# Performance work log

Hardware: AMD Instinct MI355X
Metric: run time of the kernel (lower is better)

## Reference

```python
import jax, jax.numpy as jnp
import numpy as np
import math

HEADS = 32
DIM_HEAD = 64
DM = HEADS * DIM_HEAD  # 2048
B, S = 2, 1024
BITS = 3
N_LEVELS = 2 ** BITS
N_GROUPS = (DIM_HEAD + 2) // 3  # 22
PAD = (3 - DIM_HEAD % 3) % 3    # 2
EPS_NORM = 1e-8
EPS_RMS = 1e-6


def _rotors_to_matrices(r):
    # r: (G,4) unit rotors [s, b12, b13, b23] -> (G,3,3) rotation matrices
    s, p, q, rr = r[:, 0], r[:, 1], r[:, 2], r[:, 3]
    s2, p2, q2, r2 = s * s, p * p, q * q, rr * rr
    M = np.zeros((r.shape[0], 3, 3), dtype=np.float32)
    M[:, 0, 0] = s2 - p2 - q2 + r2
    M[:, 0, 1] = 2 * s * p - 2 * q * rr
    M[:, 0, 2] = 2 * s * q + 2 * p * rr
    M[:, 1, 0] = -2 * s * p - 2 * q * rr
    M[:, 1, 1] = s2 - p2 + q2 - r2
    M[:, 1, 2] = 2 * s * rr - 2 * p * q
    M[:, 2, 0] = -2 * s * q + 2 * p * rr
    M[:, 2, 1] = -2 * s * rr - 2 * p * q
    M[:, 2, 2] = s2 + p2 - q2 - r2
    return M


def _make_compressor(seed):
    rng = np.random.default_rng(seed)
    rot = rng.standard_normal((N_GROUPS, 4)).astype(np.float32)
    rot /= np.linalg.norm(rot, axis=-1, keepdims=True)
    M = _rotors_to_matrices(rot)
    sigma = 1.0 / math.sqrt(DIM_HEAD)  # Lloyd-Max for N(0, 1/d)
    C = np.linspace(-3 * sigma, 3 * sigma, N_LEVELS, dtype=np.float32)
    return jnp.asarray(M), jnp.asarray(np.ascontiguousarray(M.transpose(0, 2, 1))), jnp.asarray(C)


def setup_inputs() -> dict:
    key = jax.random.key(0)
    ks = jax.random.split(key, 8)
    x = jax.random.normal(ks[0], (B, S, DM), dtype=jnp.float32)
    w_scale = 0.02
    Wq = jax.random.normal(ks[1], (DM, DM), dtype=jnp.float32) * w_scale
    Wk = jax.random.normal(ks[2], (DM, DM), dtype=jnp.float32) * w_scale
    Wv = jax.random.normal(ks[3], (DM, DM), dtype=jnp.float32) * w_scale
    Wo = jax.random.normal(ks[4], (DM, DM), dtype=jnp.float32) * w_scale
    qn_w = jnp.ones((DM,), dtype=jnp.float32)
    kn_w = jnp.ones((DM,), dtype=jnp.float32)
    Mk, Mtk, Ck = _make_compressor(42)
    Mv, Mtv, Cv = _make_compressor(4200)
    return {"x": x, "Wq": Wq, "Wk": Wk, "Wv": Wv, "Wo": Wo,
            "qn_w": qn_w, "kn_w": kn_w,
            "Mk": Mk, "Mtk": Mtk, "Ck": Ck,
            "Mv": Mv, "Mtv": Mtv, "Cv": Cv}


def _rmsnorm(x, w):
    return x * jax.lax.rsqrt(jnp.mean(x * x, axis=-1, keepdims=True) + EPS_RMS) * w


def _quant_roundtrip(h, M, Mt, C):
    """RotorQuant compress+decompress. h: (B,H,S,Dh) -> (B,H,S,Dh)."""
    norms = jnp.maximum(jnp.linalg.norm(h, axis=-1, keepdims=True), EPS_NORM)
    xu = h / norms
    xu = jnp.pad(xu, ((0, 0), (0, 0), (0, 0), (0, PAD)))
    g = xu.reshape(h.shape[0], h.shape[1], h.shape[2], N_GROUPS, 3)
    rot = jnp.einsum('bhsgi,gij->bhsgj', g, M)
    flat = rot.reshape(h.shape[0], h.shape[1], h.shape[2], N_GROUPS * 3)
    # nearest-centroid quantization (uint8 indices in original)
    idx = jnp.argmin(jnp.abs(flat[..., None] - C), axis=-1)
    deq = C[idx]
    g2 = deq.reshape(h.shape[0], h.shape[1], h.shape[2], N_GROUPS, 3)
    der = jnp.einsum('bhsgi,gij->bhsgj', g2, Mt)
    out = der.reshape(h.shape[0], h.shape[1], h.shape[2], N_GROUPS * 3)[..., :DIM_HEAD]
    return out * norms


def reference(x, Wq, Wk, Wv, Wo, qn_w, kn_w, Mk, Mtk, Ck, Mv, Mtv, Cv):
    b, s, _ = x.shape
    v = x @ Wv
    q = _rmsnorm(x @ Wq, qn_w)
    k = _rmsnorm(x @ Wk, kn_w)
    # split heads -> (B,H,S,Dh)
    qh = q.reshape(b, s, HEADS, DIM_HEAD).transpose(0, 2, 1, 3)
    kh = k.reshape(b, s, HEADS, DIM_HEAD).transpose(0, 2, 1, 3)
    vh = v.reshape(b, s, HEADS, DIM_HEAD).transpose(0, 2, 1, 3)
    # per-head rotor quantization roundtrip of K and V
    kh = _quant_roundtrip(kh, Mk, Mtk, Ck)
    vh = _quant_roundtrip(vh, Mv, Mtv, Cv)
    # scaled dot-product attention
    scores = jnp.einsum('bhqd,bhkd->bhqk', qh, kh) / math.sqrt(DIM_HEAD)
    probs = jax.nn.softmax(scores, axis=-1)
    o = jnp.einsum('bhqk,bhkd->bhqd', probs, vh)
    o = o.transpose(0, 2, 1, 3).reshape(b, s, DM)
    return o @ Wo
```

## Files before the change

### kernel.cpp

```cpp
#include <hip/hip_runtime.h>
#include <hip/hip_bf16.h>
#include <math.h>

#define HEADS 32
#define DIM_HEAD 64
#define DM 2048
#define BATCH 2
#define SEQ 1024
#define NROWS (BATCH * SEQ)
#define NVEC (NROWS * HEADS)
#define N_GROUPS 22
#define N_LEVELS 8
#define EPS_NORM 1e-8f
#define EPS_RMS 1e-6f

typedef float f32x4 __attribute__((ext_vector_type(4)));
typedef __bf16 bf16x8 __attribute__((ext_vector_type(8)));
typedef unsigned short u16x8 __attribute__((ext_vector_type(8)));
typedef unsigned short u16x4 __attribute__((ext_vector_type(4)));

__device__ __forceinline__ unsigned short f2bf(float x) {
  union { float f; unsigned u; } v; v.f = x;
  unsigned r = v.u + 0x7fffu + ((v.u >> 16) & 1u);
  return (unsigned short)(r >> 16);
}
__device__ __forceinline__ float bf2f(unsigned short h) {
  union { unsigned u; float f; } v; v.u = ((unsigned)h) << 16;
  return v.f;
}
__device__ __forceinline__ bf16x8 ldfrag(const unsigned short* p) {
  return __builtin_bit_cast(bf16x8, *(const u16x8*)p);
}
#define MFMA16(a, b, c) __builtin_amdgcn_mfma_f32_16x16x32_bf16((a), (b), (c), 0, 0, 0)

__device__ __forceinline__ void stage16(const unsigned short* g, unsigned short* lds) {
  __builtin_amdgcn_global_load_lds(
      (const __attribute__((address_space(1))) unsigned int*)g,
      (__attribute__((address_space(3))) unsigned int*)lds, 16, 0, 0);
}

__global__ __launch_bounds__(256) void split_convert_kernel(
    const float* __restrict__ X, unsigned short* __restrict__ hi,
    unsigned short* __restrict__ lo, int n8) {
  const int i = blockIdx.x * 256 + threadIdx.x;
  if (i >= n8) return;
  const float4 a = ((const float4*)X)[2 * i];
  const float4 b = ((const float4*)X)[2 * i + 1];
  const float v[8] = {a.x, a.y, a.z, a.w, b.x, b.y, b.z, b.w};
  u16x8 h, l;
#pragma unroll
  for (int j = 0; j < 8; ++j) {
    const unsigned short hh = f2bf(v[j]);
    h[j] = hh;
    l[j] = f2bf(v[j] - bf2f(hh));
  }
  ((u16x8*)hi)[i] = h;
  if (lo) ((u16x8*)lo)[i] = l;
}

__global__ __launch_bounds__(256) void transpose_split_batch_kernel(
    const float* __restrict__ W0, const float* __restrict__ W1,
    const float* __restrict__ W2, const float* __restrict__ W3,
    unsigned short* __restrict__ T0h, unsigned short* __restrict__ T1h,
    unsigned short* __restrict__ T1l, unsigned short* __restrict__ T2h,
    unsigned short* __restrict__ T2l, unsigned short* __restrict__ T3h) {
  const int z = blockIdx.z;
  const float* W = (z == 0) ? W0 : (z == 1) ? W1 : (z == 2) ? W2 : W3;
  unsigned short* Th = (z == 0) ? T0h : (z == 1) ? T1h : (z == 2) ? T2h : T3h;
  unsigned short* Tl = (z == 1) ? T1l : (z == 2) ? T2l : nullptr;

  __shared__ float S[64][65];
  const int t = threadIdx.x;
  const int tk = blockIdx.y * 64, tm = blockIdx.x * 64;
  {
    const int r = t >> 2, cs = (t & 3) * 16;
    const float* src = W + (size_t)(tk + r) * DM + tm + cs;
#pragma unroll
    for (int j = 0; j < 16; j += 4) {
      float4 v = *(const float4*)(src + j);
      S[r][cs + j] = v.x; S[r][cs + j + 1] = v.y;
      S[r][cs + j + 2] = v.z; S[r][cs + j + 3] = v.w;
    }
  }
  __syncthreads();
  const int m = t >> 2, ks = (t & 3) * 16;
  u16x8 h0, h1, l0, l1;
#pragma unroll
  for (int j = 0; j < 8; ++j) {
    const float v = S[ks + j][m];
    const unsigned short hh = f2bf(v);
    h0[j] = hh; l0[j] = f2bf(v - bf2f(hh));
  }
#pragma unroll
  for (int j = 0; j < 8; ++j) {
    const float v = S[ks + 8 + j][m];
    const unsigned short hh = f2bf(v);
    h1[j] = hh; l1[j] = f2bf(v - bf2f(hh));
  }
  const size_t o = (size_t)(tm + m) * DM + tk + ks;
  *(u16x8*)&Th[o] = h0; *(u16x8*)&Th[o + 8] = h1;
  if (Tl) { *(u16x8*)&Tl[o] = l0; *(u16x8*)&Tl[o + 8] = l1; }
}

__global__ __launch_bounds__(256) void qkv_gemm_kernel(
    const unsigned short* __restrict__ Ahi, const unsigned short* __restrict__ Alo,
    const unsigned short* __restrict__ Bhi, const unsigned short* __restrict__ Blo,
    float* __restrict__ q, float* __restrict__ k, float* __restrict__ v) {
  __shared__ unsigned short lAhi[128 * 32];
  __shared__ unsigned short lBhi[128 * 32];
  __shared__ unsigned short lAlo[128 * 32];
  __shared__ unsigned short lBlo[128 * 32];

  const int t = threadIdx.x;
  const int lane = t & 63, wave = t >> 6;
  const int wr = wave >> 1, wc = wave & 1;
  const int gm0 = blockIdx.y * 128;
  const int gnc = blockIdx.x * 128;
  const int seg = gnc >> 11;
  const bool split = (seg != 0);
  const int lrsub = lane >> 2;
  const int lcsub = lane & 3;

  f32x4 acc[4][4] = {};

  for (int kt = 0; kt < DM; kt += 32) {
    __syncthreads();
#pragma unroll
    for (int rg = wave; rg < 8; rg += 4) {
      const int lrow = rg * 16 + lrsub;
      const int c = lcsub ^ ((lrow >> 1) & 3);
      const size_t goffA = (size_t)(gm0 + lrow) * DM + kt + c * 8;
      const size_t goffB = (size_t)(gnc + lrow) * DM + kt + c * 8;
      stage16(Ahi + goffA, lAhi + rg * 512);
      stage16(Bhi + goffB, lBhi + rg * 512);
      if (split) {
        stage16(Alo + goffA, lAlo + rg * 512);
        stage16(Blo + goffB, lBlo + rg * 512);
      }
    }
    __syncthreads();

    bf16x8 ah[4], bh[4], al[4], bl[4];
#pragma unroll
    for (int i = 0; i < 4; ++i) {
      const int mrow = wr * 64 + i * 16 + (lane & 15);
      const int offa = mrow * 32 + (((lane >> 4) ^ ((mrow >> 1) & 3)) << 3);
      ah[i] = ldfrag(&lAhi[offa]);
      const int nrow = wc * 64 + i * 16 + (lane & 15);
      const int offb = nrow * 32 + (((lane >> 4) ^ ((nrow >> 1) & 3)) << 3);
      bh[i] = ldfrag(&lBhi[offb]);
      if (split) {
        al[i] = ldfrag(&lAlo[offa]);
        bl[i] = ldfrag(&lBlo[offb]);
      }
    }
#pragma unroll
    for (int i = 0; i < 4; ++i)
#pragma unroll
      for (int j = 0; j < 4; ++j) {
        acc[i][j] = MFMA16(ah[i], bh[j], acc[i][j]);
        if (split) {
          acc[i][j] = MFMA16(ah[i], bl[j], acc[i][j]);
          acc[i][j] = MFMA16(al[i], bh[j], acc[i][j]);
        }
      }
  }

  float* C = (seg == 0) ? q : (seg == 1) ? k : v;
  const int gn0 = gnc & 2047;
#pragma unroll
  for (int i = 0; i < 4; ++i) {
    const int row = gm0 + wr * 64 + i * 16 + ((lane >> 4) << 2);
#pragma unroll
    for (int j = 0; j < 4; ++j) {
      const int col = gn0 + wc * 64 + j * 16 + (lane & 15);
#pragma unroll
      for (int r = 0; r < 4; ++r)
        C[(size_t)(row + r) * DM + col] = acc[i][j][r];
    }
  }
}

__global__ __launch_bounds__(256) void gemm_out_splitk_kernel(
    const unsigned short* __restrict__ Ahi, const unsigned short* __restrict__ Bt,
    float* __restrict__ Cpart) {
  __shared__ unsigned short lAhi[128 * 32];
  __shared__ unsigned short lBhi[128 * 32];

  const int t = threadIdx.x;
  const int lane = t & 63, wave = t >> 6;
  const int wr = wave >> 1, wc = wave & 1;
  const int gm0 = blockIdx.y * 128, gn0 = blockIdx.x * 128;
  const int z = blockIdx.z;
  const int k0 = z * (DM / 2);
  const int lrsub = lane >> 2;
  const int lcsub = lane & 3;

  f32x4 acc[4][4] = {};

  for (int kt = k0; kt < k0 + DM / 2; kt += 32) {
    __syncthreads();
#pragma unroll
    for (int rg = wave; rg < 8; rg += 4) {
      const int lrow = rg * 16 + lrsub;
      const int c = lcsub ^ ((lrow >> 1) & 3);
      stage16(Ahi + (size_t)(gm0 + lrow) * DM + kt + c * 8, lAhi + rg * 512);
      stage16(Bt + (size_t)(gn0 + lrow) * DM + kt + c * 8, lBhi + rg * 512);
    }
    __syncthreads();

    bf16x8 ah[4], bh[4];
#pragma unroll
    for (int i = 0; i < 4; ++i) {
      const int mrow = wr * 64 + i * 16 + (lane & 15);
      ah[i] = ldfrag(&lAhi[mrow * 32 + (((lane >> 4) ^ ((mrow >> 1) & 3)) << 3)]);
      const int nrow = wc * 64 + i * 16 + (lane & 15);
      bh[i] = ldfrag(&lBhi[nrow * 32 + (((lane >> 4) ^ ((nrow >> 1) & 3)) << 3)]);
    }
#pragma unroll
    for (int i = 0; i < 4; ++i)
#pragma unroll
      for (int j = 0; j < 4; ++j)
        acc[i][j] = MFMA16(ah[i], bh[j], acc[i][j]);
  }

  float* C = Cpart + (size_t)z * NROWS * DM;
#pragma unroll
  for (int i = 0; i < 4; ++i) {
    const int row = gm0 + wr * 64 + i * 16 + ((lane >> 4) << 2);
#pragma unroll
    for (int j = 0; j < 4; ++j) {
      const int col = gn0 + wc * 64 + j * 16 + (lane & 15);
#pragma unroll
      for (int r = 0; r < 4; ++r)
        C[(size_t)(row + r) * DM + col] = acc[i][j][r];
    }
  }
}

__global__ __launch_bounds__(256) void add2_f4_kernel(
    const float* __restrict__ a, const float* __restrict__ b,
    float* __restrict__ o, int n4) {
  const int i = blockIdx.x * 256 + threadIdx.x;
  if (i >= n4) return;
  const float4 x = ((const float4*)a)[i];
  const float4 y = ((const float4*)b)[i];
  ((float4*)o)[i] = make_float4(x.x + y.x, x.y + y.y, x.z + y.z, x.w + y.w);
}

__device__ __forceinline__ float wave_sum(float x) {
#pragma unroll
  for (int o = 32; o > 0; o >>= 1) x += __shfl_xor(x, o, 64);
  return x;
}

__global__ __launch_bounds__(256) void rmsnorm_kernel(
    float* __restrict__ y, const float* __restrict__ w) {
  __shared__ float rbuf[4];
  const int row = blockIdx.x;
  float* p = y + (size_t)row * DM;
  const int t = threadIdx.x;
  const int wave = t >> 6, lane = t & 63;

  float ss = 0.f;
#pragma unroll
  for (int c = t; c < DM; c += 256) { float v = p[c]; ss += v * v; }
  ss = wave_sum(ss);
  if (lane == 0) rbuf[wave] = ss;
  __syncthreads();
  ss = rbuf[0] + rbuf[1] + rbuf[2] + rbuf[3];
  const float scale = rsqrtf(ss * (1.0f / DM) + EPS_RMS);
#pragma unroll
  for (int c = t; c < DM; c += 256) p[c] = p[c] * scale * w[c];
}

__global__ __launch_bounds__(256) void rmsnorm_split_kernel(
    const float* __restrict__ y, const float* __restrict__ w,
    unsigned short* __restrict__ hi, unsigned short* __restrict__ lo,
    float post) {
  __shared__ float rbuf[4];
  const int row = blockIdx.x;
  const float* p = y + (size_t)row * DM;
  const int t = threadIdx.x;
  const int wave = t >> 6, lane = t & 63;

  const int c0 = t * 8;
  float4 a = *(const float4*)(p + c0);
  float4 b = *(const float4*)(p + c0 + 4);
  float v[8] = {a.x, a.y, a.z, a.w, b.x, b.y, b.z, b.w};
  float ss = 0.f;
#pragma unroll
  for (int j = 0; j < 8; ++j) ss += v[j] * v[j];
  ss = wave_sum(ss);
  if (lane == 0) rbuf[wave] = ss;
  __syncthreads();
  ss = rbuf[0] + rbuf[1] + rbuf[2] + rbuf[3];
  const float scale = rsqrtf(ss * (1.0f / DM) + EPS_RMS) * post;

  u16x8 hv, lv;
#pragma unroll
  for (int j = 0; j < 8; ++j) {
    const float val = v[j] * scale * w[c0 + j];
    const unsigned short hh = f2bf(val);
    hv[j] = hh; lv[j] = f2bf(val - bf2f(hh));
  }
  *(u16x8*)&hi[(size_t)row * DM + c0] = hv;
  *(u16x8*)&lo[(size_t)row * DM + c0] = lv;
}

__device__ __forceinline__ float qnearest(float v, const float* __restrict__ C) {
  float best = C[0];
  float bd = fabsf(v - C[0]);
#pragma unroll
  for (int i = 1; i < N_LEVELS; ++i) {
    float d = fabsf(v - C[i]);
    if (d < bd) { bd = d; best = C[i]; }
  }
  return best;
}

template <bool WRITE_BF>
__global__ __launch_bounds__(256) void quant_kernel(
    float* __restrict__ kv, const float* __restrict__ M,
    const float* __restrict__ Mt, const float* __restrict__ C,
    unsigned short* __restrict__ hi, unsigned short* __restrict__ lo) {
  const int vec = blockIdx.x * blockDim.x + threadIdx.x;
  if (vec >= NVEC) return;
  float* p = kv + (size_t)vec * DIM_HEAD;

  float h[66];
  float ss = 0.f;
#pragma unroll
  for (int d = 0; d < DIM_HEAD; ++d) { h[d] = p[d]; ss += h[d] * h[d]; }
  float norm = fmaxf(sqrtf(ss), EPS_NORM);
  const float inv = 1.0f / norm;
#pragma unroll
  for (int d = 0; d < DIM_HEAD; ++d) h[d] *= inv;
  h[64] = 0.f; h[65] = 0.f;

#pragma unroll
  for (int g = 0; g < N_GROUPS; ++g) {
    const float* Mg  = M  + g * 9;
    const float* Mtg = Mt + g * 9;
    const float a0 = h[3 * g + 0], a1 = h[3 * g + 1], a2 = h[3 * g + 2];
    const float r0 = a0 * Mg[0] + a1 * Mg[3] + a2 * Mg[6];
    const float r1 = a0 * Mg[1] + a1 * Mg[4] + a2 * Mg[7];
    const float r2 = a0 * Mg[2] + a1 * Mg[5] + a2 * Mg[8];
    const float d0 = qnearest(r0, C);
    const float d1 = qnearest(r1, C);
    const float d2 = qnearest(r2, C);
    h[3 * g + 0] = d0 * Mtg[0] + d1 * Mtg[3] + d2 * Mtg[6];
    h[3 * g + 1] = d0 * Mtg[1] + d1 * Mtg[4] + d2 * Mtg[7];
    h[3 * g + 2] = d0 * Mtg[2] + d1 * Mtg[5] + d2 * Mtg[8];
  }
  if (WRITE_BF) {
#pragma unroll
    for (int g8 = 0; g8 < 8; ++g8) {
      u16x8 hv, lv;
#pragma unroll
      for (int j = 0; j < 8; ++j) {
        const float val = h[g8 * 8 + j] * norm;
        const unsigned short hh = f2bf(val);
        hv[j] = hh; lv[j] = f2bf(val - bf2f(hh));
      }
      *(u16x8*)&hi[(size_t)vec * DIM_HEAD + g8 * 8] = hv;
      *(u16x8*)&lo[(size_t)vec * DIM_HEAD + g8 * 8] = lv;
    }
  } else {
#pragma unroll
    for (int d = 0; d < DIM_HEAD; ++d) p[d] = h[d] * norm;
  }
}

__global__ __launch_bounds__(256) void vt_split_kernel(
    const float* __restrict__ v, unsigned short* __restrict__ hi,
    unsigned short* __restrict__ lo) {
  __shared__ float T[64][65];
  const int s0 = blockIdx.x * 64;
  const int bh = blockIdx.y;
  const int b = bh >> 5, h = bh & 31;
  const int t = threadIdx.x;
  {
    const int sr = t >> 2, dseg = (t & 3) * 16;
    const float* src = v + ((size_t)(b * SEQ + s0 + sr) * DM + h * 64 + dseg);
#pragma unroll
    for (int j = 0; j < 16; j += 4) {
      float4 a = *(const float4*)(src + j);
      T[sr][dseg + j] = a.x; T[sr][dseg + j + 1] = a.y;
      T[sr][dseg + j + 2] = a.z; T[sr][dseg + j + 3] = a.w;
    }
  }
  __syncthreads();
  const int d = t >> 2, sseg = (t & 3) * 16;
  u16x8 h0, h1, l0, l1;
#pragma unroll
  for (int j = 0; j < 8; ++j) {
    const float val = T[sseg + j][d];
    const unsigned short hh = f2bf(val);
    h0[j] = hh; l0[j] = f2bf(val - bf2f(hh));
  }
#pragma unroll
  for (int j = 0; j < 8; ++j) {
    const float val = T[sseg + 8 + j][d];
    const unsigned short hh = f2bf(val);
    h1[j] = hh; l1[j] = f2bf(val - bf2f(hh));
  }
  const size_t o = (size_t)(bh * 64 + d) * SEQ + s0 + sseg;
  *(u16x8*)&hi[o] = h0; *(u16x8*)&hi[o + 8] = h1;
  *(u16x8*)&lo[o] = l0; *(u16x8*)&lo[o + 8] = l1;
}

__global__ __launch_bounds__(256) void attn_mfma_kernel(
    const unsigned short* __restrict__ qhi, const unsigned short* __restrict__ qlo,
    const unsigned short* __restrict__ khi, const unsigned short* __restrict__ klo,
    const unsigned short* __restrict__ vthi, const unsigned short* __restrict__ vtlo,
    unsigned short* __restrict__ ohi) {
  __shared__ unsigned short Ks_h[4096], Ks_l[4096];
  __shared__ unsigned short Vt_h[4096], Vt_l[4096];
  __shared__ unsigned int   Ps[4096];

  const int bh = blockIdx.x;
  const int qt = blockIdx.y;
  const int h = bh & 31, b = bh >> 5;
  const int q0 = qt * 64;
  const int t = threadIdx.x, lane = t & 63, w = t >> 6;
  const int quad = lane >> 4, l15 = lane & 15;
  const int srow = lane >> 3, schunk = lane & 7;

  auto stage = [&](const unsigned short* g, int stride, unsigned short* arr) {
#pragma unroll
    for (int it = 0; it < 2; ++it) {
      const int r = w * 16 + it * 8 + srow;
      const int c = schunk ^ (r & 7);
      stage16(g + (size_t)r * stride + c * 8, arr + (w * 16 + it * 8) * 64);
    }
  };

  bf16x8 qh[2], ql[2];
  {
    const size_t qrow = (size_t)(b * SEQ + q0 + w * 16 + l15) * DM + h * 64;
#pragma unroll
    for (int ks = 0; ks < 2; ++ks) {
      qh[ks] = ldfrag(&qhi[qrow + ks * 32 + quad * 8]);
      ql[ks] = ldfrag(&qlo[qrow + ks * 32 + quad * 8]);
    }
  }

  f32x4 acc[4] = {};
  float m_prev[4] = {-INFINITY, -INFINITY, -INFINITY, -INFINITY};
  float lsum[4] = {0.f, 0.f, 0.f, 0.f};

  const unsigned short* gkh = khi + ((size_t)(b * SEQ) * DM + h * 64);
  const unsigned short* gkl = klo + ((size_t)(b * SEQ) * DM + h * 64);
  const unsigned short* gvh = vthi + (size_t)(bh * 64) * SEQ;
  const unsigned short* gvl = vtlo + (size_t)(bh * 64) * SEQ;

  for (int kt = 0; kt < SEQ; kt += 64) {
    __syncthreads();
    stage(gkh + (size_t)kt * DM, DM, Ks_h);
    stage(gkl + (size_t)kt * DM, DM, Ks_l);
    stage(gvh + kt, SEQ, Vt_h);
    stage(gvl + kt, SEQ, Vt_l);
    __syncthreads();

    f32x4 s[4] = {};
#pragma unroll
    for (int nt = 0; nt < 4; ++nt) {
#pragma unroll
      for (int ks = 0; ks < 2; ++ks) {
        const int row = nt * 16 + l15;
        const int off = row * 64 + (((quad + 4 * ks) ^ (row & 7)) << 3);
        const bf16x8 kh = ldfrag(&Ks_h[off]);
        const bf16x8 kl = ldfrag(&Ks_l[off]);
        s[nt] = MFMA16(qh[ks], kh, s[nt]);
        s[nt] = MFMA16(qh[ks], kl, s[nt]);
        s[nt] = MFMA16(ql[ks], kh, s[nt]);
      }
    }

    float asave[4];
#pragma unroll
    for (int r = 0; r < 4; ++r) {
      float mx = fmaxf(fmaxf(s[0][r], s[1][r]), fmaxf(s[2][r], s[3][r]));
#pragma unroll
      for (int off = 1; off < 16; off <<= 1) mx = fmaxf(mx, __shfl_xor(mx, off, 64));
      const float mn = fmaxf(m_prev[r], mx);
      const float al = __expf(m_prev[r] - mn);
      float rs = 0.f;
#pragma unroll
      for (int nt = 0; nt < 4; ++nt) {
        const float e = __expf(s[nt][r] - mn);
        s[nt][r] = e; rs += e;
      }
#pragma unroll
      for (int off = 1; off < 16; off <<= 1) rs += __shfl_xor(rs, off, 64);
      lsum[r] = lsum[r] * al + rs;
      m_prev[r] = mn;
      asave[r] = al;
      const int prow = w * 16 + quad * 4 + r;
#pragma unroll
      for (int nt = 0; nt < 4; ++nt) {
        const int kk = nt * 16 + l15;
        const unsigned short hh = f2bf(s[nt][r]);
        const unsigned short ll = f2bf(s[nt][r] - bf2f(hh));
        Ps[prow * 64 + (kk ^ ((prow & 7) << 3))] =
            ((unsigned)hh << 16) | (unsigned)ll;
      }
    }

    {
      const int src = (l15 >> 2) << 4;
      const float a0 = __shfl(asave[0], src, 64);
      const float a1 = __shfl(asave[1], src, 64);
      const float a2 = __shfl(asave[2], src, 64);
      const float a3 = __shfl(asave[3], src, 64);
      const int rr = l15 & 3;
      const float alph = (rr == 0) ? a0 : (rr == 1) ? a1 : (rr == 2) ? a2 : a3;
#pragma unroll
      for (int mt = 0; mt < 4; ++mt) acc[mt] *= alph;
    }

    bf16x8 ph[2], pl[2];
#pragma unroll
    for (int ks = 0; ks < 2; ++ks) {
      const int prow = w * 16 + l15;
      const unsigned int* pp =
          &Ps[prow * 64 + ((ks * 32 + quad * 8) ^ ((prow & 7) << 3))];
      const uint4 pa = *(const uint4*)pp;
      const uint4 pb = *(const uint4*)(pp + 4);
      u16x8 hv, lv;
      const unsigned int pw[8] = {pa.x, pa.y, pa.z, pa.w, pb.x, pb.y, pb.z, pb.w};
#pragma unroll
      for (int j = 0; j < 8; ++j) {
        hv[j] = (unsigned short)(pw[j] >> 16);
        lv[j] = (unsigned short)(pw[j] & 0xffffu);
      }
      ph[ks] = __builtin_bit_cast(bf16x8, hv);
      pl[ks] = __builtin_bit_cast(bf16x8, lv);
    }

#pragma unroll
    for (int mt = 0; mt < 4; ++mt) {
#pragma unroll
      for (int ks = 0; ks < 2; ++ks) {
        const int drow = mt * 16 + l15;
        const int offv = drow * 64 + (((quad + 4 * ks) ^ (drow & 7)) << 3);
        const bf16x8 vh = ldfrag(&Vt_h[offv]);
        const bf16x8 vl = ldfrag(&Vt_l[offv]);
        acc[mt] = MFMA16(vh, ph[ks], acc[mt]);
        acc[mt] = MFMA16(vh, pl[ks], acc[mt]);
        acc[mt] = MFMA16(vl, ph[ks], acc[mt]);
      }
    }
  }

  {
    const int src = (l15 >> 2) << 4;
    const float a0 = __shfl(lsum[0], src, 64);
    const float a1 = __shfl(lsum[1], src, 64);
    const float a2 = __shfl(lsum[2], src, 64);
    const float a3 = __shfl(lsum[3], src, 64);
    const int rr = l15 & 3;
    const float lq = (rr == 0) ? a0 : (rr == 1) ? a1 : (rr == 2) ? a2 : a3;
    const float inv = 1.0f / lq;
    const size_t obase = (size_t)(b * SEQ + q0 + w * 16 + l15) * DM + h * 64;
#pragma unroll
    for (int mt = 0; mt < 4; ++mt) {
      u16x4 ov;
#pragma unroll
      for (int r = 0; r < 4; ++r) ov[r] = f2bf(acc[mt][r] * inv);
      *(u16x4*)&ohi[obase + mt * 16 + quad * 4] = ov;
    }
  }
}

extern "C" void kernel_launch(void* const* d_in, const int* in_sizes, int n_in,
                              void* d_out, int out_size, void* d_ws, size_t ws_size,
                              hipStream_t stream) {
  const float* x    = (const float*)d_in[0];
  const float* Wq   = (const float*)d_in[1];
  const float* Wk   = (const float*)d_in[2];
  const float* Wv   = (const float*)d_in[3];
  const float* Wo   = (const float*)d_in[4];
  const float* qn_w = (const float*)d_in[5];
  const float* kn_w = (const float*)d_in[6];
  const float* Mk   = (const float*)d_in[7];
  const float* Mtk  = (const float*)d_in[8];
  const float* Ck   = (const float*)d_in[9];
  const float* Mv   = (const float*)d_in[10];
  const float* Mtv  = (const float*)d_in[11];
  const float* Cv   = (const float*)d_in[12];
  float* out = (float*)d_out;

  const size_t MBb = 1024ull * 1024ull;
  const size_t SEG = (size_t)DM * DM;
  char* w = (char*)d_ws;
  float* qb = (float*)(w + 0 * MBb);
  float* kb = (float*)(w + 16 * MBb);
  float* vb = (float*)(w + 32 * MBb);
  unsigned short* xhi     = (unsigned short*)(w + 48 * MBb);
  unsigned short* xlo     = (unsigned short*)(w + 56 * MBb);
  unsigned short* wcat_hi = (unsigned short*)(w + 64 * MBb);
  unsigned short* wcat_lo = (unsigned short*)(w + 88 * MBb);
  unsigned short* wot     = (unsigned short*)(w + 112 * MBb);
  unsigned short* q_hi  = wcat_hi;
  unsigned short* k_hi  = wcat_hi + SEG;
  unsigned short* k_lo  = wcat_hi + 2 * SEG;
  unsigned short* q_lo  = wcat_lo;
  unsigned short* vt_hi = wcat_lo + SEG;
  unsigned short* vt_lo = wcat_lo + 2 * SEG;
  unsigned short* o_hi  = xhi;
  float* opart = (float*)(w + 0 * MBb);

  const int n8 = (NROWS * DM) / 8;

  split_convert_kernel<<<n8 / 256, 256, 0, stream>>>(x, xhi, xlo, n8);
  transpose_split_batch_kernel<<<dim3(DM / 64, DM / 64, 4), 256, 0, stream>>>(
      Wq, Wk, Wv, Wo,
      wcat_hi, wcat_hi + SEG, wcat_lo + SEG, wcat_hi + 2 * SEG, wcat_lo + 2 * SEG, wot);

  qkv_gemm_kernel<<<dim3(3 * DM / 128, NROWS / 128), 256, 0, stream>>>(
      xhi, xlo, wcat_hi, wcat_lo, qb, kb, vb);

  rmsnorm_kernel<<<NROWS, 256, 0, stream>>>(kb, kn_w);
  rmsnorm_split_kernel<<<NROWS, 256, 0, stream>>>(qb, qn_w, q_hi, q_lo, 0.125f);

  quant_kernel<true ><<<NVEC / 256, 256, 0, stream>>>(kb, Mk, Mtk, Ck, k_hi, k_lo);
  quant_kernel<false><<<NVEC / 256, 256, 0, stream>>>(vb, Mv, Mtv, Cv, nullptr, nullptr);
  vt_split_kernel<<<dim3(SEQ / 64, BATCH * HEADS), 256, 0, stream>>>(vb, vt_hi, vt_lo);

  attn_mfma_kernel<<<dim3(BATCH * HEADS, SEQ / 64), 256, 0, stream>>>(
      q_hi, q_lo, k_hi, k_lo, vt_hi, vt_lo, o_hi);

  gemm_out_splitk_kernel<<<dim3(DM / 128, NROWS / 128, 2), 256, 0, stream>>>(
      o_hi, wot, opart);
  add2_f4_kernel<<<(NROWS * DM / 4 + 255) / 256, 256, 0, stream>>>(
      opart, opart + (size_t)NROWS * DM, out, NROWS * DM / 4);
}
```

Before: 458.8 us.

## Rewrite QKV and output GEMMs with double-buffered async LDS pipeline and 8 waves

Replaces the QKV and output-projection GEMMs with new kernels that use 512-thread blocks (8 waves), a 64-wide K tile, and double-buffered LDS. The next tile is prefetched with global_load_lds while the current one is computed, using explicit vmcnt waits, barriers and raised wave priority around the MFMA block. The fused QKV launch is split into a plain-bf16 Q GEMM and a separate split-precision K/V GEMM that stages its hi/lo operands in phases. The aim is to hide global-load latency and drop the per-block branching on the split path. The cost is a larger LDS footprint, which may limit occupancy, and hand-written wait counts that must match the loads actually issued.

```diff
diff --git a/kernel.cpp b/kernel.cpp
--- a/kernel.cpp
+++ b/kernel.cpp
@@ -39,6 +39,11 @@
       (__attribute__((address_space(3))) unsigned int*)lds, 16, 0, 0);
 }
 
+#define WAITV(N) asm volatile("s_waitcnt vmcnt(" #N ")" ::: "memory")
+#define WAITL0() asm volatile("s_waitcnt lgkmcnt(0)" ::: "memory")
+#define SBARM()  asm volatile("s_barrier" ::: "memory")
+#define SFENCE() __builtin_amdgcn_sched_barrier(0)
+
 __global__ __launch_bounds__(256) void split_convert_kernel(
     const float* __restrict__ X, unsigned short* __restrict__ hi,
     unsigned short* __restrict__ lo, int n8) {
@@ -102,135 +107,176 @@
   if (Tl) { *(u16x8*)&Tl[o] = l0; *(u16x8*)&Tl[o + 8] = l1; }
 }
 
-__global__ __launch_bounds__(256) void qkv_gemm_kernel(
-    const unsigned short* __restrict__ Ahi, const unsigned short* __restrict__ Alo,
-    const unsigned short* __restrict__ Bhi, const unsigned short* __restrict__ Blo,
-    float* __restrict__ q, float* __restrict__ k, float* __restrict__ v) {
-  __shared__ unsigned short lAhi[128 * 32];
-  __shared__ unsigned short lBhi[128 * 32];
-  __shared__ unsigned short lAlo[128 * 32];
-  __shared__ unsigned short lBlo[128 * 32];
-
-  const int t = threadIdx.x;
-  const int lane = t & 63, wave = t >> 6;
-  const int wr = wave >> 1, wc = wave & 1;
+__global__ __launch_bounds__(512, 2) void gemm_plain8(
+    const unsigned short* __restrict__ A, const unsigned short* __restrict__ B,
+    float* __restrict__ C, int ntiles) {
+  __shared__ unsigned short L[2][2][128 * 64];
+  const int t = threadIdx.x, lane = t & 63, w = t >> 6;
+  const int wr = w >> 2, wc = w & 3;
   const int gm0 = blockIdx.y * 128;
-  const int gnc = blockIdx.x * 128;
-  const int seg = gnc >> 11;
-  const bool split = (seg != 0);
-  const int lrsub = lane >> 2;
-  const int lcsub = lane & 3;
-
-  f32x4 acc[4][4] = {};
-
-  for (int kt = 0; kt < DM; kt += 32) {
-    __syncthreads();
-#pragma unroll
-    for (int rg = wave; rg < 8; rg += 4) {
-      const int lrow = rg * 16 + lrsub;
-      const int c = lcsub ^ ((lrow >> 1) & 3);
-      const size_t goffA = (size_t)(gm0 + lrow) * DM + kt + c * 8;
-      const size_t goffB = (size_t)(gnc + lrow) * DM + kt + c * 8;
-      stage16(Ahi + goffA, lAhi + rg * 512);
-      stage16(Bhi + goffB, lBhi + rg * 512);
-      if (split) {
-        stage16(Alo + goffA, lAlo + rg * 512);
-        stage16(Blo + goffB, lBlo + rg * 512);
-      }
-    }
-    __syncthreads();
-
-    bf16x8 ah[4], bh[4], al[4], bl[4];
-#pragma unroll
-    for (int i = 0; i < 4; ++i) {
-      const int mrow = wr * 64 + i * 16 + (lane & 15);
-      const int offa = mrow * 32 + (((lane >> 4) ^ ((mrow >> 1) & 3)) << 3);
-      ah[i] = ldfrag(&lAhi[offa]);
-      const int nrow = wc * 64 + i * 16 + (lane & 15);
-      const int offb = nrow * 32 + (((lane >> 4) ^ ((nrow >> 1) & 3)) << 3);
-      bh[i] = ldfrag(&lBhi[offb]);
-      if (split) {
-        al[i] = ldfrag(&lAlo[offa]);
-        bl[i] = ldfrag(&lBlo[offb]);
-      }
-    }
+  const int gn0 = blockIdx.x * 128;
+  const int z = blockIdx.z;
+  const int k0 = z * (ntiles << 6);
+  const int chunk = (lane & 7) ^ (lane >> 3);
+
+  auto stg = [&](const unsigned short* g, int row0, int kt, unsigned short* dst) {
+#pragma unroll
+    for (int it = 0; it < 2; ++it) {
+      const int r = (w << 4) + (it << 3) + (lane >> 3);
+      stage16(g + (size_t)(row0 + r) * DM + kt + chunk * 8,
+              dst + ((w << 4) + (it << 3)) * 64);
+    }
+  };
+
+  f32x4 acc[4][2] = {};
+
+  stg(A, gm0, k0, L[0][0]);
+  stg(B, gn0, k0, L[0][1]);
+
+  for (int tt = 0; tt < ntiles; ++tt) {
+    const int c = tt & 1, n = c ^ 1;
+    const bool pf = (tt + 1 < ntiles);
+    if (pf) {
+      const int ktn = k0 + ((tt + 1) << 6);
+      stg(A, gm0, ktn, L[n][0]);
+      stg(B, gn0, ktn, L[n][1]);
+      WAITV(4);
+    } else {
+      WAITV(0);
+    }
+    SBARM(); SFENCE();
+    const unsigned short* cA = L[c][0];
+    const unsigned short* cB = L[c][1];
+    bf16x8 fa[4][2], fb[2][2];
+#pragma unroll
+    for (int ks = 0; ks < 2; ++ks) {
+      const int ch = ks * 4 + (lane >> 4);
+#pragma unroll
+      for (int i = 0; i < 4; ++i) {
+        const int row = wr * 64 + i * 16 + (lane & 15);
+        fa[i][ks] = ldfrag(&cA[row * 64 + ((ch ^ (row & 7)) << 3)]);
+      }
+#pragma unroll
+      for (int j = 0; j < 2; ++j) {
+        const int row = wc * 32 + j * 16 + (lane & 15);
+        fb[j][ks] = ldfrag(&cB[row * 64 + ((ch ^ (row & 7)) << 3)]);
+      }
+    }
+    WAITL0();
+    __builtin_amdgcn_s_setprio(1);
 #pragma unroll
     for (int i = 0; i < 4; ++i)
 #pragma unroll
-      for (int j = 0; j < 4; ++j) {
-        acc[i][j] = MFMA16(ah[i], bh[j], acc[i][j]);
-        if (split) {
-          acc[i][j] = MFMA16(ah[i], bl[j], acc[i][j]);
-          acc[i][j] = MFMA16(al[i], bh[j], acc[i][j]);
-        }
-      }
-  }
-
-  float* C = (seg == 0) ? q : (seg == 1) ? k : v;
-  const int gn0 = gnc & 2047;
+      for (int j = 0; j < 2; ++j)
+#pragma unroll
+        for (int ks = 0; ks < 2; ++ks)
+          acc[i][j] = MFMA16(fa[i][ks], fb[j][ks], acc[i][j]);
+    __builtin_amdgcn_s_setprio(0);
+    SFENCE(); SBARM();
+  }
+
+  float* Cz = C + (size_t)z * NROWS * DM;
 #pragma unroll
   for (int i = 0; i < 4; ++i) {
     const int row = gm0 + wr * 64 + i * 16 + ((lane >> 4) << 2);
 #pragma unroll
-    for (int j = 0; j < 4; ++j) {
-      const int col = gn0 + wc * 64 + j * 16 + (lane & 15);
+    for (int j = 0; j < 2; ++j) {
+      const int col = gn0 + wc * 32 + j * 16 + (lane & 15);
 #pragma unroll
       for (int r = 0; r < 4; ++r)
-        C[(size_t)(row + r) * DM + col] = acc[i][j][r];
-    }
-  }
-}
-
-__global__ __launch_bounds__(256) void gemm_out_splitk_kernel(
-    const unsigned short* __restrict__ Ahi, const unsigned short* __restrict__ Bt,
-    float* __restrict__ Cpart) {
-  __shared__ unsigned short lAhi[128 * 32];
-  __shared__ unsigned short lBhi[128 * 32];
-
-  const int t = threadIdx.x;
-  const int lane = t & 63, wave = t >> 6;
-  const int wr = wave >> 1, wc = wave & 1;
-  const int gm0 = blockIdx.y * 128, gn0 = blockIdx.x * 128;
-  const int z = blockIdx.z;
-  const int k0 = z * (DM / 2);
-  const int lrsub = lane >> 2;
-  const int lcsub = lane & 3;
-
-  f32x4 acc[4][4] = {};
-
-  for (int kt = k0; kt < k0 + DM / 2; kt += 32) {
-    __syncthreads();
-#pragma unroll
-    for (int rg = wave; rg < 8; rg += 4) {
-      const int lrow = rg * 16 + lrsub;
-      const int c = lcsub ^ ((lrow >> 1) & 3);
-      stage16(Ahi + (size_t)(gm0 + lrow) * DM + kt + c * 8, lAhi + rg * 512);
-      stage16(Bt + (size_t)(gn0 + lrow) * DM + kt + c * 8, lBhi + rg * 512);
-    }
-    __syncthreads();
-
-    bf16x8 ah[4], bh[4];
-#pragma unroll
-    for (int i = 0; i < 4; ++i) {
-      const int mrow = wr * 64 + i * 16 + (lane & 15);
-      ah[i] = ldfrag(&lAhi[mrow * 32 + (((lane >> 4) ^ ((mrow >> 1) & 3)) << 3)]);
-      const int nrow = wc * 64 + i * 16 + (lane & 15);
-      bh[i] = ldfrag(&lBhi[nrow * 32 + (((lane >> 4) ^ ((nrow >> 1) & 3)) << 3)]);
-    }
+        Cz[(size_t)(row + r) * DM + col] = acc[i][j][r];
+    }
+  }
+}
+
+__global__ __launch_bounds__(512, 2) void gemm_kv_split8(
+    const unsigned short* __restrict__ Ah, const unsigned short* __restrict__ Al,
+    const unsigned short* __restrict__ Bh, const unsigned short* __restrict__ Bl,
+    float* __restrict__ kout, float* __restrict__ vout) {
+  __shared__ unsigned short L[2][4][128 * 64];
+  const int t = threadIdx.x, lane = t & 63, w = t >> 6;
+  const int wr = w >> 2, wc = w & 3;
+  const int gm0 = blockIdx.y * 128;
+  const int nAbs = 2048 + blockIdx.x * 128;
+  const int seg = nAbs >> 11;
+  const int gn0 = nAbs & 2047;
+  const int chunk = (lane & 7) ^ (lane >> 3);
+
+  auto stg = [&](const unsigned short* g, int row0, int kt, unsigned short* dst) {
+#pragma unroll
+    for (int it = 0; it < 2; ++it) {
+      const int r = (w << 4) + (it << 3) + (lane >> 3);
+      stage16(g + (size_t)(row0 + r) * DM + kt + chunk * 8,
+              dst + ((w << 4) + (it << 3)) * 64);
+    }
+  };
+
+  f32x4 acc[4][2] = {};
+
+  auto group = [&](const unsigned short* arrA, const unsigned short* arrB) {
+    bf16x8 fa[4][2], fb[2][2];
+#pragma unroll
+    for (int ks = 0; ks < 2; ++ks) {
+      const int ch = ks * 4 + (lane >> 4);
+#pragma unroll
+      for (int i = 0; i < 4; ++i) {
+        const int row = wr * 64 + i * 16 + (lane & 15);
+        fa[i][ks] = ldfrag(&arrA[row * 64 + ((ch ^ (row & 7)) << 3)]);
+      }
+#pragma unroll
+      for (int j = 0; j < 2; ++j) {
+        const int row = wc * 32 + j * 16 + (lane & 15);
+        fb[j][ks] = ldfrag(&arrB[row * 64 + ((ch ^ (row & 7)) << 3)]);
+      }
+    }
+    WAITL0();
+    __builtin_amdgcn_s_setprio(1);
 #pragma unroll
     for (int i = 0; i < 4; ++i)
 #pragma unroll
-      for (int j = 0; j < 4; ++j)
-        acc[i][j] = MFMA16(ah[i], bh[j], acc[i][j]);
-  }
-
-  float* C = Cpart + (size_t)z * NROWS * DM;
+      for (int j = 0; j < 2; ++j)
+#pragma unroll
+        for (int ks = 0; ks < 2; ++ks)
+          acc[i][j] = MFMA16(fa[i][ks], fb[j][ks], acc[i][j]);
+    __builtin_amdgcn_s_setprio(0);
+  };
+
+  stg(Ah, gm0, 0, L[0][0]);
+  stg(Bh, nAbs, 0, L[0][1]);
+  stg(Bl, nAbs, 0, L[0][2]);
+  stg(Al, gm0, 0, L[0][3]);
+
+  for (int tt = 0; tt < 32; ++tt) {
+    const int c = tt & 1, n = c ^ 1;
+    const bool pf = (tt + 1 < 32);
+    const int ktn = (tt + 1) << 6;
+
+    if (pf) { stg(Ah, gm0, ktn, L[n][0]); stg(Bh, nAbs, ktn, L[n][1]); WAITV(8); }
+    else WAITV(4);
+    SBARM(); SFENCE();
+    group(L[c][0], L[c][1]);
+    SFENCE(); SBARM();
+
+    if (pf) { stg(Bl, nAbs, ktn, L[n][2]); WAITV(8); }
+    else WAITV(2);
+    SBARM(); SFENCE();
+    group(L[c][0], L[c][2]);
+    SFENCE(); SBARM();
+
+    if (pf) { stg(Al, gm0, ktn, L[n][3]); WAITV(8); }
+    else WAITV(0);
+    SBARM(); SFENCE();
+    group(L[c][3], L[c][1]);
+    SFENCE(); SBARM();
+  }
+
+  float* C = (seg == 1) ? kout : vout;
 #pragma unroll
   for (int i = 0; i < 4; ++i) {
     const int row = gm0 + wr * 64 + i * 16 + ((lane >> 4) << 2);
 #pragma unroll
-    for (int j = 0; j < 4; ++j) {
-      const int col = gn0 + wc * 64 + j * 16 + (lane & 15);
+    for (int j = 0; j < 2; ++j) {
+      const int col = gn0 + wc * 32 + j * 16 + (lane & 15);
 #pragma unroll
       for (int r = 0; r < 4; ++r)
         C[(size_t)(row + r) * DM + col] = acc[i][j][r];
@@ -619,8 +665,10 @@
       Wq, Wk, Wv, Wo,
       wcat_hi, wcat_hi + SEG, wcat_lo + SEG, wcat_hi + 2 * SEG, wcat_lo + 2 * SEG, wot);
 
-  qkv_gemm_kernel<<<dim3(3 * DM / 128, NROWS / 128), 256, 0, stream>>>(
-      xhi, xlo, wcat_hi, wcat_lo, qb, kb, vb);
+  gemm_plain8<<<dim3(DM / 128, NROWS / 128, 1), 512, 0, stream>>>(
+      xhi, wcat_hi, qb, DM / 64);
+  gemm_kv_split8<<<dim3(2 * DM / 128, NROWS / 128), 512, 0, stream>>>(
+      xhi, xlo, wcat_hi, wcat_lo, kb, vb);
 
   rmsnorm_kernel<<<NROWS, 256, 0, stream>>>(kb, kn_w);
   rmsnorm_split_kernel<<<NROWS, 256, 0, stream>>>(qb, qn_w, q_hi, q_lo, 0.125f);
@@ -632,8 +680,8 @@
   attn_mfma_kernel<<<dim3(BATCH * HEADS, SEQ / 64), 256, 0, stream>>>(
       q_hi, q_lo, k_hi, k_lo, vt_hi, vt_lo, o_hi);
 
-  gemm_out_splitk_kernel<<<dim3(DM / 128, NROWS / 128, 2), 256, 0, stream>>>(
-      o_hi, wot, opart);
+  gemm_plain8<<<dim3(DM / 128, NROWS / 128, 2), 512, 0, stream>>>(
+      o_hi, wot, opart, DM / 64 / 2);
   add2_f4_kernel<<<(NROWS * DM / 4 + 255) / 256, 256, 0, stream>>>(
       opart, opart + (size_t)NROWS * DM, out, NROWS * DM / 4);
 }
```

New measurement: 481.9 us. 5.0% more time.

## Double-buffer K/V tiles in attention kernel with async prefetch and setprio

Applied to the files above, without the earlier changes.

The attention kernel now double-buffers the K/V LDS tiles, issuing global_load_lds for the next tile before computing on the current one. Raw s_waitcnt vmcnt and s_barrier replace the two __syncthreads per iteration, with sched_barrier fences around them. s_setprio is raised around the MFMA blocks. The goal is to hide global-load latency behind compute, at the cost of doubling LDS use (about 80KB), which may reduce occupancy. The vmcnt(8) count depends on the exact number of outstanding loads, which makes it fragile.

```diff
diff --git a/kernel.cpp b/kernel.cpp
--- a/kernel.cpp
+++ b/kernel.cpp
@@ -38,6 +38,10 @@
       (const __attribute__((address_space(1))) unsigned int*)g,
       (__attribute__((address_space(3))) unsigned int*)lds, 16, 0, 0);
 }
+
+#define WAITV(N) asm volatile("s_waitcnt vmcnt(" #N ")" ::: "memory")
+#define SBARM()  asm volatile("s_barrier" ::: "memory")
+#define SFENCE() __builtin_amdgcn_sched_barrier(0)
 
 __global__ __launch_bounds__(256) void split_convert_kernel(
     const float* __restrict__ X, unsigned short* __restrict__ hi,
@@ -415,8 +419,8 @@
     const unsigned short* __restrict__ khi, const unsigned short* __restrict__ klo,
     const unsigned short* __restrict__ vthi, const unsigned short* __restrict__ vtlo,
     unsigned short* __restrict__ ohi) {
-  __shared__ unsigned short Ks_h[4096], Ks_l[4096];
-  __shared__ unsigned short Vt_h[4096], Vt_l[4096];
+  __shared__ unsigned short Ks_h[2][4096], Ks_l[2][4096];
+  __shared__ unsigned short Vt_h[2][4096], Vt_l[2][4096];
   __shared__ unsigned int   Ps[4096];
 
   const int bh = blockIdx.x;
@@ -436,47 +440,64 @@
     }
   };
 
-  bf16x8 qh[2], ql[2];
-  {
-    const size_t qrow = (size_t)(b * SEQ + q0 + w * 16 + l15) * DM + h * 64;
-#pragma unroll
-    for (int ks = 0; ks < 2; ++ks) {
-      qh[ks] = ldfrag(&qhi[qrow + ks * 32 + quad * 8]);
-      ql[ks] = ldfrag(&qlo[qrow + ks * 32 + quad * 8]);
-    }
-  }
-
-  f32x4 acc[4] = {};
-  float m_prev[4] = {-INFINITY, -INFINITY, -INFINITY, -INFINITY};
-  float lsum[4] = {0.f, 0.f, 0.f, 0.f};
-
   const unsigned short* gkh = khi + ((size_t)(b * SEQ) * DM + h * 64);
   const unsigned short* gkl = klo + ((size_t)(b * SEQ) * DM + h * 64);
   const unsigned short* gvh = vthi + (size_t)(bh * 64) * SEQ;
   const unsigned short* gvl = vtlo + (size_t)(bh * 64) * SEQ;
 
-  for (int kt = 0; kt < SEQ; kt += 64) {
-    __syncthreads();
-    stage(gkh + (size_t)kt * DM, DM, Ks_h);
-    stage(gkl + (size_t)kt * DM, DM, Ks_l);
-    stage(gvh + kt, SEQ, Vt_h);
-    stage(gvl + kt, SEQ, Vt_l);
-    __syncthreads();
+  auto stageAll = [&](int kt, int buf) {
+    stage(gkh + (size_t)kt * DM, DM, Ks_h[buf]);
+    stage(gkl + (size_t)kt * DM, DM, Ks_l[buf]);
+    stage(gvh + kt, SEQ, Vt_h[buf]);
+    stage(gvl + kt, SEQ, Vt_l[buf]);
+  };
+
+  bf16x8 qh[2], ql[2];
+  {
+    const size_t qrow = (size_t)(b * SEQ + q0 + w * 16 + l15) * DM + h * 64;
+#pragma unroll
+    for (int ks = 0; ks < 2; ++ks) {
+      qh[ks] = ldfrag(&qhi[qrow + ks * 32 + quad * 8]);
+      ql[ks] = ldfrag(&qlo[qrow + ks * 32 + quad * 8]);
+    }
+  }
+
+  f32x4 acc[4] = {};
+  float m_prev[4] = {-INFINITY, -INFINITY, -INFINITY, -INFINITY};
+  float lsum[4] = {0.f, 0.f, 0.f, 0.f};
+
+  stageAll(0, 0);
+
+  for (int tt = 0; tt < 16; ++tt) {
+    const int c = tt & 1, n = c ^ 1;
+    if (tt < 15) {
+      stageAll((tt + 1) * 64, n);
+      WAITV(8);
+    } else {
+      WAITV(0);
+    }
+    SBARM(); SFENCE();
+    const unsigned short* cKh = Ks_h[c];
+    const unsigned short* cKl = Ks_l[c];
+    const unsigned short* cVh = Vt_h[c];
+    const unsigned short* cVl = Vt_l[c];
 
     f32x4 s[4] = {};
+    __builtin_amdgcn_s_setprio(1);
 #pragma unroll
     for (int nt = 0; nt < 4; ++nt) {
 #pragma unroll
       for (int ks = 0; ks < 2; ++ks) {
         const int row = nt * 16 + l15;
         const int off = row * 64 + (((quad + 4 * ks) ^ (row & 7)) << 3);
-        const bf16x8 kh = ldfrag(&Ks_h[off]);
-        const bf16x8 kl = ldfrag(&Ks_l[off]);
+        const bf16x8 kh = ldfrag(&cKh[off]);
+        const bf16x8 kl = ldfrag(&cKl[off]);
         s[nt] = MFMA16(qh[ks], kh, s[nt]);
         s[nt] = MFMA16(qh[ks], kl, s[nt]);
         s[nt] = MFMA16(ql[ks], kh, s[nt]);
       }
     }
+    __builtin_amdgcn_s_setprio(0);
 
     float asave[4];
 #pragma unroll
@@ -539,19 +560,22 @@
       pl[ks] = __builtin_bit_cast(bf16x8, lv);
     }
 
+    __builtin_amdgcn_s_setprio(1);
 #pragma unroll
     for (int mt = 0; mt < 4; ++mt) {
 #pragma unroll
       for (int ks = 0; ks < 2; ++ks) {
         const int drow = mt * 16 + l15;
         const int offv = drow * 64 + (((quad + 4 * ks) ^ (drow & 7)) << 3);
-        const bf16x8 vh = ldfrag(&Vt_h[offv]);
-        const bf16x8 vl = ldfrag(&Vt_l[offv]);
+        const bf16x8 vh = ldfrag(&cVh[offv]);
+        const bf16x8 vl = ldfrag(&cVl[offv]);
         acc[mt] = MFMA16(vh, ph[ks], acc[mt]);
         acc[mt] = MFMA16(vh, pl[ks], acc[mt]);
         acc[mt] = MFMA16(vl, ph[ks], acc[mt]);
       }
     }
+    __builtin_amdgcn_s_setprio(0);
+    SFENCE(); SBARM();
   }
 
   {
```

Measured after the change: 461.1 us. About the same (+0.5%).
